# Performance work log

Measured on AMD Instinct MI355X. Metric: run time of the kernel, lower is better.

The kernel has to match this reference:

```python
import jax, jax.numpy as jnp
import numpy as np

B, N, F, C = 8, 256, 59, 128
BOX = 20.0
EPS = 1e-5


def _bn(y, g, b, m, v):
    # eval-mode BatchNorm1d over the channel (last) axis
    return (y - m) * jax.lax.rsqrt(v + EPS) * g + b


def setup_inputs() -> dict:
    key = jax.random.key(0)
    ks = jax.random.split(key, 12)
    x = jax.random.normal(ks[0], (B, N, F), jnp.float32)
    pos = jax.random.uniform(ks[1], (B, N, 3), jnp.float32) * BOX
    nrm = jax.random.normal(ks[2], (B, N, 3), jnp.float32)
    normal = nrm / jnp.linalg.norm(nrm, axis=-1, keepdims=True)
    s_in = 1.0 / np.sqrt(F)
    W_lin = jax.random.normal(ks[3], (C, F), jnp.float32) * s_in
    W_src = jax.random.normal(ks[4], (C, F), jnp.float32) * s_in
    W_dst = jax.random.normal(ks[5], (C, F), jnp.float32) * s_in
    pos_w = jax.random.normal(ks[6], (C, 6), jnp.float32) * (1.0 / np.sqrt(6.0))
    pos_b = jax.random.normal(ks[7], (C,), jnp.float32) * 0.02
    attn_w = jax.random.normal(ks[8], (C, C), jnp.float32) * (1.0 / np.sqrt(C))
    attn_b = jax.random.normal(ks[9], (C,), jnp.float32) * 0.02
    pos_bn_g = 1.0 + 0.1 * jax.random.normal(ks[10], (C,), jnp.float32)
    attn_bn_g = 1.0 + 0.1 * jax.random.normal(ks[11], (C,), jnp.float32)
    zeros = jnp.zeros((C,), jnp.float32)
    ones = jnp.ones((C,), jnp.float32)
    return {
        'x': x, 'pos': pos, 'normal': normal,
        'W_lin': W_lin, 'W_src': W_src, 'W_dst': W_dst,
        'pos_w': pos_w, 'pos_b': pos_b,
        'pos_bn_g': pos_bn_g, 'pos_bn_b': zeros, 'pos_bn_m': zeros, 'pos_bn_v': ones,
        'attn_w': attn_w, 'attn_b': attn_b,
        'attn_bn_g': attn_bn_g, 'attn_bn_b': zeros, 'attn_bn_m': zeros, 'attn_bn_v': ones,
        'r': 5,
    }


def reference(x, pos, normal, W_lin, W_src, W_dst, pos_w, pos_b,
              pos_bn_g, pos_bn_b, pos_bn_m, pos_bn_v,
              attn_w, attn_b, attn_bn_g, attn_bn_b, attn_bn_m, attn_bn_v, r):
    r = jnp.float32(r)
    # linear projections (bias-free, as in PyG PointTransformerConv)
    v = jnp.einsum('bnf,cf->bnc', x, W_lin)      # values
    a_src = jnp.einsum('bnf,cf->bnc', x, W_src)  # alpha for source j
    a_dst = jnp.einsum('bnf,cf->bnc', x, W_dst)  # alpha for dest   i
    # relative geometry, axis 1 = receiver i, axis 2 = sender j
    rel_pos = pos[:, :, None, :] - pos[:, None, :, :]          # [B,i,j,3]
    rel_nrm = normal[:, :, None, :] - normal[:, None, :, :]    # [B,i,j,3]
    relf = jnp.concatenate([rel_pos, rel_nrm], axis=-1)        # [B,i,j,6]
    # pos_nn = Linear(6,C) + BN + ReLU (eval)
    delta = jax.nn.relu(_bn(jnp.einsum('bijk,ck->bijc', relf, pos_w) + pos_b,
                            pos_bn_g, pos_bn_b, pos_bn_m, pos_bn_v))
    # attn_nn(alpha_i - alpha_j + delta)
    alpha_arg = a_dst[:, :, None, :] - a_src[:, None, :, :] + delta
    scores = jax.nn.relu(_bn(jnp.einsum('bijc,dc->bijd', alpha_arg, attn_w) + attn_b,
                             attn_bn_g, attn_bn_b, attn_bn_m, attn_bn_v))
    # radius mask within each graph (self-loops included, dist 0 <= r)
    dist2 = jnp.sum(rel_pos * rel_pos, axis=-1)                # [B,i,j]
    mask = (dist2 <= r * r)[..., None]                         # [B,i,j,1]
    attn = jax.nn.softmax(jnp.where(mask, scores, -jnp.inf), axis=2)
    # per-channel vector attention over neighbors j: sum_j attn * (v_j + delta)
    out = jnp.sum(attn * (v[:, None, :, :] + delta), axis=2)   # [B,i,C]
    return out
```

## Files before the change

kernel.cpp:

```cpp
#include <hip/hip_runtime.h>

typedef _Float16 h2 __attribute__((ext_vector_type(2)));
typedef unsigned int uint32;

#define BB 8
#define NN 256
#define FF 59
#define CC 128
#define EPSV 1e-5f

#define WS_V     0
#define WS_ASRC  (WS_V + BB*NN*CC)
#define WS_ADST  (WS_ASRC + BB*NN*CC)
#define WS_PWT   (WS_ADST + BB*NN*CC)
#define WS_T1    (WS_PWT + 6*CC)
#define WS_T2    (WS_T1 + CC)
#define WS_WTH   (WS_T2 + CC)

#if __has_builtin(__builtin_amdgcn_fdot2)
#define FDOT2(a, b, c) __builtin_amdgcn_fdot2((a), (b), (c), false)
#else
static __device__ __forceinline__ float fdot2_emul(h2 a, h2 b, float c) {
    return c + (float)a.x * (float)b.x + (float)a.y * (float)b.y;
}
#define FDOT2 fdot2_emul
#endif

static __device__ __forceinline__ h2 as_h2(uint32 u) {
    return __builtin_bit_cast(h2, u);
}

__global__ __launch_bounds__(256) void prep_kernel(
    const float* __restrict__ x, const float* __restrict__ W_lin,
    const float* __restrict__ W_src, const float* __restrict__ W_dst,
    const float* __restrict__ pos_w, const float* __restrict__ pos_b,
    const float* __restrict__ pos_g, const float* __restrict__ pos_bb,
    const float* __restrict__ pos_m, const float* __restrict__ pos_v,
    const float* __restrict__ attn_w, const float* __restrict__ attn_b,
    const float* __restrict__ attn_g, const float* __restrict__ attn_bb,
    const float* __restrict__ attn_m, const float* __restrict__ attn_v,
    float* __restrict__ ws)
{
    int blk = blockIdx.x;
    int tid = threadIdx.x;
    if (blk < 768) {
        int type = blk >> 8;
        int g    = blk & 255;
        int b    = g >> 5;
        int n0   = (g & 31) * 8;
        const float* W = (type == 0) ? W_lin : (type == 1) ? W_src : W_dst;
        float* outp = ws + ((type == 0) ? WS_V : (type == 1) ? WS_ASRC : WS_ADST);
        __shared__ float Wl[CC * 60];
        __shared__ float xs[8 * 60];
        for (int idx = tid; idx < CC * 60; idx += 256) {
            int r = idx / 60, f = idx - r * 60;
            Wl[idx] = (f < FF) ? W[r * FF + f] : 0.f;
        }
        const float* xrow = x + (size_t)(b * NN + n0) * FF;
        for (int idx = tid; idx < 8 * 60; idx += 256) {
            int r = idx / 60, f = idx - r * 60;
            xs[idx] = (f < FF) ? xrow[r * FF + f] : 0.f;
        }
        __syncthreads();
        int c = tid & 127, h = tid >> 7;
        float acc[4];
#pragma unroll
        for (int q = 0; q < 4; ++q) acc[q] = 0.f;
#pragma unroll 3
        for (int f4 = 0; f4 < 15; ++f4) {
            float4 wq = *(const float4*)&Wl[c * 60 + f4 * 4];
#pragma unroll
            for (int q = 0; q < 4; ++q) {
                float4 xq = *(const float4*)&xs[(h * 4 + q) * 60 + f4 * 4];
                acc[q] = fmaf(wq.x, xq.x, acc[q]);
                acc[q] = fmaf(wq.y, xq.y, acc[q]);
                acc[q] = fmaf(wq.z, xq.z, acc[q]);
                acc[q] = fmaf(wq.w, xq.w, acc[q]);
            }
        }
#pragma unroll
        for (int q = 0; q < 4; ++q) {
            int n = n0 + h * 4 + q;
            outp[(b * NN + n) * CC + c] = acc[q];
        }
    } else {
        __shared__ float S2s[CC];
        if (tid < CC) {
            int c = tid;
            float S1 = rsqrtf(pos_v[c] + EPSV) * pos_g[c];
            ws[WS_T1 + c] = (pos_b[c] - pos_m[c]) * S1 + pos_bb[c];
#pragma unroll
            for (int k = 0; k < 6; ++k) ws[WS_PWT + k * CC + c] = pos_w[c * 6 + k] * S1;
            float S2 = rsqrtf(attn_v[c] + EPSV) * attn_g[c];
            S2s[c] = S2;
            ws[WS_T2 + c] = (attn_b[c] - attn_m[c]) * S2 + attn_bb[c];
        }
        __syncthreads();
        uint32* wthp = (uint32*)ws + WS_WTH;
        for (int idx = tid; idx < 64 * CC; idx += 256) {
            int p = idx & 63, d = idx >> 6;
            float s = S2s[d];
            float2 w2 = *(const float2*)&attn_w[d * CC + 2 * p];
            h2 hv;
            hv.x = (_Float16)(w2.x * s);
            hv.y = (_Float16)(w2.y * s);
            wthp[p * CC + d] = __builtin_bit_cast(uint32, hv);
        }
    }
}

__global__ __launch_bounds__(256, 6) void main_kernel(
    const float* __restrict__ pos, const float* __restrict__ nrm,
    const int* __restrict__ rptr, const float* __restrict__ ws,
    float* __restrict__ out)
{
    const float* v    = ws + WS_V;
    const float* asrc = ws + WS_ASRC;
    const float* adst = ws + WS_ADST;
    const float* pwt  = ws + WS_PWT;
    const float* T1   = ws + WS_T1;
    const float* T2   = ws + WS_T2;
    const uint32* wth = (const uint32*)ws + WS_WTH;

    int blk = blockIdx.x;
    int b = blk >> 8, i = blk & 255;
    int tid = threadIdx.x;

    __shared__ float relf[NN * 6];
    __shared__ int   jlist[NN];
    __shared__ int   wcnt[4];
    __shared__ int   cnt_s;
    __shared__ _Float16 alpha_h[16 * 136];
    __shared__ float sered[CC], ored[CC];

    int rv = rptr[0];
    float r2 = (float)(rv * rv);
    const float* pib = pos + (size_t)(b * NN + i) * 3;
    const float* nib = nrm + (size_t)(b * NN + i) * 3;
    float pix = pib[0], piy = pib[1], piz = pib[2];
    float nix = nib[0], niy = nib[1], niz = nib[2];
    {
        int j = tid;
        const float* pj = pos + (size_t)(b * NN + j) * 3;
        const float* nj = nrm + (size_t)(b * NN + j) * 3;
        float dx = pix - pj[0], dy = piy - pj[1], dz = piz - pj[2];
        float ex = nix - nj[0], ey = niy - nj[1], ez = niz - nj[2];
        float d2 = dx * dx + dy * dy + dz * dz;
        bool valid = (d2 <= r2);
        unsigned long long m = __ballot(valid);
        int w = tid >> 6, lane = tid & 63;
        if (lane == 0) wcnt[w] = __popcll(m);
        __syncthreads();
        int off = 0;
        for (int w2 = 0; w2 < w; ++w2) off += wcnt[w2];
        if (tid == 0) cnt_s = wcnt[0] + wcnt[1] + wcnt[2] + wcnt[3];
        int rank = __popcll(m & ((1ull << lane) - 1ull));
        if (valid) {
            int s = off + rank;
            jlist[s] = j;
            relf[s * 6 + 0] = dx; relf[s * 6 + 1] = dy; relf[s * 6 + 2] = dz;
            relf[s * 6 + 3] = ex; relf[s * 6 + 4] = ey; relf[s * 6 + 5] = ez;
        }
    }
    __syncthreads();
    int cnt = cnt_s;

    int c    = tid & 127;
    int half = tid >> 7;

    float pw[6];
#pragma unroll
    for (int k = 0; k < 6; ++k) pw[k] = pwt[k * CC + c];
    float T1c    = T1[c];
    float T2d    = T2[c];
    float adst_c = adst[(b * NN + i) * CC + c];

    float se = 0.f, ov = 0.f;

    for (int base = 0; base < cnt; base += 16) {
        int tcnt = min(16, cnt - base);
        int myn  = tcnt - half * 8;
        float u_reg[8];
#pragma unroll
        for (int q = 0; q < 8; ++q) {
            float aval = 0.f;
            u_reg[q] = 0.f;
            if (q < myn) {
                int js = base + half * 8 + q;
                int j  = jlist[js];
                const float2* rp = (const float2*)&relf[js * 6];
                float2 r0 = rp[0], r1 = rp[1], r2f = rp[2];
                float dsum = T1c;
                dsum = fmaf(pw[0], r0.x, dsum);
                dsum = fmaf(pw[1], r0.y, dsum);
                dsum = fmaf(pw[2], r1.x, dsum);
                dsum = fmaf(pw[3], r1.y, dsum);
                dsum = fmaf(pw[4], r2f.x, dsum);
                dsum = fmaf(pw[5], r2f.y, dsum);
                float delta = fmaxf(dsum, 0.f);
                aval = adst_c - asrc[(b * NN + j) * CC + c] + delta;
                u_reg[q] = v[(b * NN + j) * CC + c] + delta;
            }
            alpha_h[(half * 8 + q) * 136 + c] = (_Float16)aval;
        }
        __syncthreads();
        if (myn > 0) {
            float acc[8];
#pragma unroll
            for (int q = 0; q < 8; ++q) acc[q] = T2d;
            const uint32* wp = wth + c;
#pragma unroll 4
            for (int co = 0; co < 16; ++co) {
                uint32 w0 = wp[(co * 4 + 0) * CC];
                uint32 w1 = wp[(co * 4 + 1) * CC];
                uint32 w2 = wp[(co * 4 + 2) * CC];
                uint32 w3 = wp[(co * 4 + 3) * CC];
                h2 h0 = as_h2(w0), h1 = as_h2(w1), hh2 = as_h2(w2), h3 = as_h2(w3);
#pragma unroll
                for (int q = 0; q < 8; ++q) {
                    uint4 av = *(const uint4*)&alpha_h[(half * 8 + q) * 136 + co * 8];
                    acc[q] = FDOT2(as_h2(av.x), h0, acc[q]);
                    acc[q] = FDOT2(as_h2(av.y), h1, acc[q]);
                    acc[q] = FDOT2(as_h2(av.z), hh2, acc[q]);
                    acc[q] = FDOT2(as_h2(av.w), h3, acc[q]);
                }
            }
#pragma unroll
            for (int q = 0; q < 8; ++q) {
                if (q < myn) {
                    float s = fmaxf(acc[q], 0.f);
                    float e = __expf(s);
                    se += e;
                    ov += e * u_reg[q];
                }
            }
        }
        __syncthreads();
    }

    if (half == 1) { sered[c] = se; ored[c] = ov; }
    __syncthreads();
    if (half == 0) {
        float S = se + sered[c];
        float O = ov + ored[c];
        out[(size_t)(b * NN + i) * CC + c] = O / S;
    }
}

extern "C" void kernel_launch(void* const* d_in, const int* in_sizes, int n_in,
                              void* d_out, int out_size, void* d_ws, size_t ws_size,
                              hipStream_t stream) {
    const float* x      = (const float*)d_in[0];
    const float* pos    = (const float*)d_in[1];
    const float* normal = (const float*)d_in[2];
    const float* W_lin  = (const float*)d_in[3];
    const float* W_src  = (const float*)d_in[4];
    const float* W_dst  = (const float*)d_in[5];
    const float* pos_w  = (const float*)d_in[6];
    const float* pos_b  = (const float*)d_in[7];
    const float* pos_g  = (const float*)d_in[8];
    const float* pos_bb = (const float*)d_in[9];
    const float* pos_m  = (const float*)d_in[10];
    const float* pos_v  = (const float*)d_in[11];
    const float* attn_w = (const float*)d_in[12];
    const float* attn_b = (const float*)d_in[13];
    const float* attn_g = (const float*)d_in[14];
    const float* attn_bb= (const float*)d_in[15];
    const float* attn_m = (const float*)d_in[16];
    const float* attn_v = (const float*)d_in[17];
    const int*   rptr   = (const int*)d_in[18];
    float* ws  = (float*)d_ws;
    float* out = (float*)d_out;

    prep_kernel<<<dim3(769), dim3(256), 0, stream>>>(
        x, W_lin, W_src, W_dst, pos_w, pos_b, pos_g, pos_bb, pos_m, pos_v,
        attn_w, attn_b, attn_g, attn_bb, attn_m, attn_v, ws);
    main_kernel<<<dim3(2048), dim3(256), 0, stream>>>(pos, normal, rptr, ws, out);
}
```

Before: 126.8 us.

## Replace fdot2 attention projection with MFMA 16x16x32 f16 matrix ops

The per-neighbor 128x128 attention projection now runs on 16x16x32 f16 MFMA instructions instead of scalar fdot2 loops. Weights are pre-swizzled in the prep kernel into the MFMA B-fragment layout and held in registers for the whole block. The value+delta terms are staged in LDS so each lane can read the entries matching its MFMA output layout, and the final reduction uses cross-lane shuffles instead of LDS. Launch bounds drop from 6 to 4 blocks per CU to make room for the register-resident weight fragments, which may lower occupancy.

```diff
diff --git a/kernel.cpp b/kernel.cpp
--- a/kernel.cpp
+++ b/kernel.cpp
@@ -1,6 +1,8 @@
 #include <hip/hip_runtime.h>
 
 typedef _Float16 h2 __attribute__((ext_vector_type(2)));
+typedef _Float16 f16x8 __attribute__((ext_vector_type(8)));
+typedef float f32x4 __attribute__((ext_vector_type(4)));
 typedef unsigned int uint32;
 
 #define BB 8
@@ -15,20 +17,7 @@
 #define WS_PWT   (WS_ADST + BB*NN*CC)
 #define WS_T1    (WS_PWT + 6*CC)
 #define WS_T2    (WS_T1 + CC)
-#define WS_WTH   (WS_T2 + CC)
-
-#if __has_builtin(__builtin_amdgcn_fdot2)
-#define FDOT2(a, b, c) __builtin_amdgcn_fdot2((a), (b), (c), false)
-#else
-static __device__ __forceinline__ float fdot2_emul(h2 a, h2 b, float c) {
-    return c + (float)a.x * (float)b.x + (float)a.y * (float)b.y;
-}
-#define FDOT2 fdot2_emul
-#endif
-
-static __device__ __forceinline__ h2 as_h2(uint32 u) {
-    return __builtin_bit_cast(h2, u);
-}
+#define WS_WTB   (WS_T2 + CC)
 
 __global__ __launch_bounds__(256) void prep_kernel(
     const float* __restrict__ x, const float* __restrict__ W_lin,
@@ -96,20 +85,31 @@
             ws[WS_T2 + c] = (attn_b[c] - attn_m[c]) * S2 + attn_bb[c];
         }
         __syncthreads();
-        uint32* wthp = (uint32*)ws + WS_WTH;
-        for (int idx = tid; idx < 64 * CC; idx += 256) {
-            int p = idx & 63, d = idx >> 6;
-            float s = S2s[d];
-            float2 w2 = *(const float2*)&attn_w[d * CC + 2 * p];
-            h2 hv;
-            hv.x = (_Float16)(w2.x * s);
-            hv.y = (_Float16)(w2.y * s);
-            wthp[p * CC + d] = __builtin_bit_cast(uint32, hv);
+        uint4* wtbp = (uint4*)(ws + WS_WTB);
+        for (int idx = tid; idx < 32 * 64; idx += 256) {
+            int l = idx & 63, ts = idx >> 6;
+            int t = ts >> 2, s = ts & 3;
+            int d  = t * 16 + (l & 15);
+            int c0 = s * 32 + ((l >> 4) << 3);
+            float S2 = S2s[d];
+            float4 w0 = *(const float4*)&attn_w[d * CC + c0];
+            float4 w1 = *(const float4*)&attn_w[d * CC + c0 + 4];
+            h2 p0, p1, p2, p3;
+            p0.x = (_Float16)(w0.x * S2); p0.y = (_Float16)(w0.y * S2);
+            p1.x = (_Float16)(w0.z * S2); p1.y = (_Float16)(w0.w * S2);
+            p2.x = (_Float16)(w1.x * S2); p2.y = (_Float16)(w1.y * S2);
+            p3.x = (_Float16)(w1.z * S2); p3.y = (_Float16)(w1.w * S2);
+            uint4 o;
+            o.x = __builtin_bit_cast(uint32, p0);
+            o.y = __builtin_bit_cast(uint32, p1);
+            o.z = __builtin_bit_cast(uint32, p2);
+            o.w = __builtin_bit_cast(uint32, p3);
+            wtbp[idx] = o;
         }
     }
 }
 
-__global__ __launch_bounds__(256, 6) void main_kernel(
+__global__ __launch_bounds__(256, 4) void main_kernel(
     const float* __restrict__ pos, const float* __restrict__ nrm,
     const int* __restrict__ rptr, const float* __restrict__ ws,
     float* __restrict__ out)
@@ -120,7 +120,6 @@
     const float* pwt  = ws + WS_PWT;
     const float* T1   = ws + WS_T1;
     const float* T2   = ws + WS_T2;
-    const uint32* wth = (const uint32*)ws + WS_WTH;
 
     int blk = blockIdx.x;
     int b = blk >> 8, i = blk & 255;
@@ -131,7 +130,7 @@
     __shared__ int   wcnt[4];
     __shared__ int   cnt_s;
     __shared__ _Float16 alpha_h[16 * 136];
-    __shared__ float sered[CC], ored[CC];
+    __shared__ float    u_lds[16 * 136];
 
     int rv = rptr[0];
     float r2 = (float)(rv * rv);
@@ -167,24 +166,36 @@
 
     int c    = tid & 127;
     int half = tid >> 7;
+    int w    = tid >> 6;
+    int lane = tid & 63;
+
+    f16x8 bf[2][4];
+    {
+        const uint4* wtb = (const uint4*)(ws + WS_WTB);
+#pragma unroll
+        for (int tt = 0; tt < 2; ++tt)
+#pragma unroll
+            for (int s = 0; s < 4; ++s)
+                bf[tt][s] = __builtin_bit_cast(f16x8,
+                    wtb[((w * 2 + tt) * 4 + s) * 64 + lane]);
+    }
+    float T2a = T2[w * 32 + (lane & 15)];
+    float T2b = T2[w * 32 + 16 + (lane & 15)];
 
     float pw[6];
 #pragma unroll
     for (int k = 0; k < 6; ++k) pw[k] = pwt[k * CC + c];
     float T1c    = T1[c];
-    float T2d    = T2[c];
     float adst_c = adst[(b * NN + i) * CC + c];
 
-    float se = 0.f, ov = 0.f;
+    float pse0 = 0.f, pov0 = 0.f, pse1 = 0.f, pov1 = 0.f;
 
     for (int base = 0; base < cnt; base += 16) {
         int tcnt = min(16, cnt - base);
         int myn  = tcnt - half * 8;
-        float u_reg[8];
 #pragma unroll
         for (int q = 0; q < 8; ++q) {
-            float aval = 0.f;
-            u_reg[q] = 0.f;
+            float aval = 0.f, uval = 0.f;
             if (q < myn) {
                 int js = base + half * 8 + q;
                 int j  = jlist[js];
@@ -199,51 +210,48 @@
                 dsum = fmaf(pw[5], r2f.y, dsum);
                 float delta = fmaxf(dsum, 0.f);
                 aval = adst_c - asrc[(b * NN + j) * CC + c] + delta;
-                u_reg[q] = v[(b * NN + j) * CC + c] + delta;
+                uval = v[(b * NN + j) * CC + c] + delta;
             }
             alpha_h[(half * 8 + q) * 136 + c] = (_Float16)aval;
-        }
-        __syncthreads();
-        if (myn > 0) {
-            float acc[8];
-#pragma unroll
-            for (int q = 0; q < 8; ++q) acc[q] = T2d;
-            const uint32* wp = wth + c;
-#pragma unroll 4
-            for (int co = 0; co < 16; ++co) {
-                uint32 w0 = wp[(co * 4 + 0) * CC];
-                uint32 w1 = wp[(co * 4 + 1) * CC];
-                uint32 w2 = wp[(co * 4 + 2) * CC];
-                uint32 w3 = wp[(co * 4 + 3) * CC];
-                h2 h0 = as_h2(w0), h1 = as_h2(w1), hh2 = as_h2(w2), h3 = as_h2(w3);
-#pragma unroll
-                for (int q = 0; q < 8; ++q) {
-                    uint4 av = *(const uint4*)&alpha_h[(half * 8 + q) * 136 + co * 8];
-                    acc[q] = FDOT2(as_h2(av.x), h0, acc[q]);
-                    acc[q] = FDOT2(as_h2(av.y), h1, acc[q]);
-                    acc[q] = FDOT2(as_h2(av.z), hh2, acc[q]);
-                    acc[q] = FDOT2(as_h2(av.w), h3, acc[q]);
-                }
-            }
-#pragma unroll
-            for (int q = 0; q < 8; ++q) {
-                if (q < myn) {
-                    float s = fmaxf(acc[q], 0.f);
-                    float e = __expf(s);
-                    se += e;
-                    ov += e * u_reg[q];
-                }
-            }
-        }
-        __syncthreads();
-    }
-
-    if (half == 1) { sered[c] = se; ored[c] = ov; }
-    __syncthreads();
-    if (half == 0) {
-        float S = se + sered[c];
-        float O = ov + ored[c];
-        out[(size_t)(b * NN + i) * CC + c] = O / S;
+            u_lds[(half * 8 + q) * 136 + c]  = uval;
+        }
+        __syncthreads();
+        f32x4 acc0 = {T2a, T2a, T2a, T2a};
+        f32x4 acc1 = {T2b, T2b, T2b, T2b};
+        {
+            const _Float16* arow = &alpha_h[(lane & 15) * 136 + ((lane >> 4) << 3)];
+#pragma unroll
+            for (int s = 0; s < 4; ++s) {
+                f16x8 af = *(const f16x8*)(arow + s * 32);
+                acc0 = __builtin_amdgcn_mfma_f32_16x16x32_f16(af, bf[0][s], acc0, 0, 0, 0);
+                acc1 = __builtin_amdgcn_mfma_f32_16x16x32_f16(af, bf[1][s], acc1, 0, 0, 0);
+            }
+        }
+        {
+            int d0 = w * 32 + (lane & 15);
+#pragma unroll
+            for (int rg = 0; rg < 4; ++rg) {
+                int j = ((lane >> 4) << 2) + rg;
+                bool jvalid = (j < tcnt);
+                float e0 = jvalid ? __expf(fmaxf(acc0[rg], 0.f)) : 0.f;
+                float e1 = jvalid ? __expf(fmaxf(acc1[rg], 0.f)) : 0.f;
+                pse0 += e0;
+                pov0 += e0 * u_lds[j * 136 + d0];
+                pse1 += e1;
+                pov1 += e1 * u_lds[j * 136 + d0 + 16];
+            }
+        }
+        __syncthreads();
+    }
+
+    pse0 += __shfl_xor(pse0, 16); pse0 += __shfl_xor(pse0, 32);
+    pov0 += __shfl_xor(pov0, 16); pov0 += __shfl_xor(pov0, 32);
+    pse1 += __shfl_xor(pse1, 16); pse1 += __shfl_xor(pse1, 32);
+    pov1 += __shfl_xor(pov1, 16); pov1 += __shfl_xor(pov1, 32);
+    if (lane < 16) {
+        size_t o = (size_t)(b * NN + i) * CC + w * 32 + lane;
+        out[o]      = pov0 / pse0;
+        out[o + 16] = pov1 / pse1;
     }
 }
 
```

New measurement: 114.6 us. 9.6% less time.
